# Kernel optimization log

Measured on AMD Instinct MI355X. Metric: run time of the kernel, lower is better.

## Reference

```python
import jax, jax.numpy as jnp
import numpy as np

N = 100000
E = 1600000


def _gcn_conv(x, src, dst, norm, W, b, n_nodes):
    # PyG GCNConv: h = x @ W; aggregate normalized messages; add bias.
    h = x @ W                                   # [N, C_out]
    msg = h[src] * norm[:, None]                # [E', C_out] gathered messages
    out = jax.ops.segment_sum(msg, dst, num_segments=n_nodes)
    return out + b


def _norm_coeffs(src, dst, n_nodes):
    # symmetric normalization with self-loops: D^{-1/2} (A+I) D^{-1/2}
    ones = jnp.ones(src.shape[0], dtype=jnp.float32)
    deg = jax.ops.segment_sum(ones, dst, num_segments=n_nodes)
    dis = jnp.where(deg > 0, jax.lax.rsqrt(jnp.maximum(deg, 1.0)), 0.0)
    return dis[src] * dis[dst]


def setup_inputs() -> dict:
    key = jax.random.key(0)
    k1, k2, k3, k4 = jax.random.split(key, 4)
    x = jax.random.normal(k1, (N, 128), dtype=jnp.float32)
    edge_index = jax.random.randint(k2, (2, E), 0, N, dtype=jnp.int64)
    W1 = jax.random.normal(k3, (128, 128), dtype=jnp.float32) * (1.0 / np.sqrt(128))
    b1 = jnp.zeros((128,), dtype=jnp.float32)
    W2 = jax.random.normal(k4, (128, 64), dtype=jnp.float32) * (1.0 / np.sqrt(128))
    b2 = jnp.zeros((64,), dtype=jnp.float32)
    return {"x": x, "edge_index": edge_index, "W1": W1, "b1": b1, "W2": W2, "b2": b2}


def reference(x, edge_index, W1, b1, W2, b2):
    n_nodes = x.shape[0]
    loop = jnp.arange(n_nodes, dtype=edge_index.dtype)
    src = jnp.concatenate([edge_index[0], loop])   # add self-loops
    dst = jnp.concatenate([edge_index[1], loop])
    norm = _norm_coeffs(src, dst, n_nodes)
    h = _gcn_conv(x, src, dst, norm, W1, b1, n_nodes)
    h = jax.nn.relu(h)
    # dropout(p=0.2) is identity in eval mode
    out = _gcn_conv(h, src, dst, norm, W2, b2, n_nodes)
    return out
```

## Files before the change

kernel.cpp:

```cpp
#include <hip/hip_runtime.h>
#include <hip/hip_bf16.h>


typedef short short8v __attribute__((ext_vector_type(8)));
typedef float f32x4   __attribute__((ext_vector_type(4)));
typedef int   int4v   __attribute__((ext_vector_type(4)));

#define BSHIFT 9
#define BSIZE  512
#define CAPSH  14
#define CAP    (1 << CAPSH)
#define IDXCAP 4096

__device__ __forceinline__ short f2bf(float f) {
    unsigned u = __float_as_uint(f);
    return (short)((u + 0x7fffu + ((u >> 16) & 1u)) >> 16);
}
__device__ __forceinline__ unsigned pack2bf(float a, float b) {
    return (unsigned)(unsigned short)f2bf(a) | ((unsigned)(unsigned short)f2bf(b) << 16);
}
__device__ __forceinline__ float bflo(unsigned u) { return __uint_as_float(u << 16); }
__device__ __forceinline__ float bfhi(unsigned u) { return __uint_as_float(u & 0xffff0000u); }

__global__ void k_prep(const float* __restrict__ W1, const float* __restrict__ W2,
                       short* __restrict__ w1t, short* __restrict__ w2t,
                       int* __restrict__ bcur, int nbuck,
                       short* __restrict__ bufH, short* __restrict__ bufH2, int N) {
    int b = blockIdx.x;
    int t = threadIdx.x;
    if (b == gridDim.x - 1) {
        if (t < nbuck) bcur[t] = t << CAPSH;
        size_t np1 = (size_t)N + 1;
        if (t < 128) {
            bufH[((size_t)(t >> 4) * np1 + N) * 16 + (t & 15)] = 0;
        } else if (t < 192) {
            int z = t - 128;
            bufH2[((size_t)(z >> 4) * np1 + N) * 16 + (z & 15)] = 0;
        }
        return;
    }
    int i = b * 256 + t;
    if (i < 128 * 128) {
        int n = i >> 7, k = i & 127;
        w1t[i] = f2bf(W1[k * 128 + n]);
    } else {
        int j = i - 128 * 128;
        int n = j >> 7, k = j & 127;
        w2t[j] = f2bf(W2[k * 64 + n]);
    }
}

__global__ __launch_bounds__(256) void k_bucket(const int* __restrict__ src,
                                                const int* __restrict__ dst,
                                                int* __restrict__ bcur,
                                                unsigned* __restrict__ ebuf,
                                                int E, int nbuck) {
    __shared__ int sdst[4096];
    __shared__ int ssrc[4096];
    __shared__ int hist[256];
    __shared__ int base[256];
    int t = threadIdx.x;
    int e0 = blockIdx.x * 4096;
    for (int i = t; i < nbuck; i += 256) hist[i] = 0;
    for (int i = 0; i < 16; ++i) {
        int k = i * 256 + t;
        int e = e0 + k;
        sdst[k] = (e < E) ? dst[e] : -1;
        ssrc[k] = (e < E) ? src[e] : 0;
    }
    __syncthreads();
    for (int i = 0; i < 16; ++i) {
        int d = sdst[i * 256 + t];
        if (d >= 0) atomicAdd(&hist[d >> BSHIFT], 1);
    }
    __syncthreads();
    for (int b = t; b < nbuck; b += 256) {
        int c = hist[b];
        base[b] = c ? atomicAdd(&bcur[b], c) : 0;
        hist[b] = 0;
    }
    __syncthreads();
    for (int i = 0; i < 16; ++i) {
        int k = i * 256 + t;
        int d = sdst[k];
        if (d >= 0) {
            int bk = d >> BSHIFT;
            int off = atomicAdd(&hist[bk], 1);
            ebuf[base[bk] + off] = ((unsigned)ssrc[k] << BSHIFT) | (unsigned)(d & (BSIZE - 1));
        }
    }
}

__global__ __launch_bounds__(BSIZE) void k_bcsr(const unsigned* __restrict__ ebuf,
                                                const int* __restrict__ bcur,
                                                float* __restrict__ dinv,
                                                int* __restrict__ nord,
                                                int* __restrict__ degr,
                                                int* __restrict__ rpr,
                                                unsigned* __restrict__ csr4, int n) {
    __shared__ unsigned edges[CAP];
    __shared__ int hist[BSIZE];
    __shared__ int s[BSIZE];
    __shared__ int cur[BSIZE];
    int b = blockIdx.x;
    int t = threadIdx.x;
    hist[t] = 0;
    __syncthreads();
    int base = b << CAPSH;
    int cnt  = bcur[b] - base;
    int lo = b << BSHIFT;
    for (int k = t; k < cnt; k += BSIZE) {
        unsigned e = ebuf[base + k];
        edges[k] = e;
        atomicAdd(&hist[e & (BSIZE - 1)], 1);
    }
    __syncthreads();
    int v = hist[t];
    int node = lo + t;
    bool valid = node < n;
    __syncthreads();
    hist[t] = 0;
    __syncthreads();
    int key = valid ? min(v, BSIZE - 1) : 0;
    atomicAdd(&hist[key], 1);
    __syncthreads();
    s[t] = hist[t];
    __syncthreads();
    for (int off = 1; off < BSIZE; off <<= 1) {
        int add = (t >= off) ? s[t - off] : 0;
        __syncthreads();
        s[t] += add;
        __syncthreads();
    }
    cur[t] = 0;
    __syncthreads();
    int r = (s[key] - hist[key]) + atomicAdd(&cur[key], 1);
    __syncthreads();
    int pv = valid ? ((v + 4) & ~3) : 0;
    s[r] = pv;
    __syncthreads();
    for (int off = 1; off < BSIZE; off <<= 1) {
        int add = (t >= off) ? s[t - off] : 0;
        __syncthreads();
        s[t] += add;
        __syncthreads();
    }
    int rp = base + s[r] - pv;
    cur[t] = rp + 1;
    int slot = (b << BSHIFT) + r;
    if (valid) {
        dinv[node] = rsqrtf((float)(v + 1));
        nord[slot] = node;
        degr[slot] = v;
        rpr[slot]  = rp;
        csr4[rp] = (unsigned)node;
        for (int j = v + 1; j < pv; ++j) csr4[rp + j] = (unsigned)n;
    } else {
        nord[slot] = -1;
        degr[slot] = 0;
        rpr[slot]  = rp;
    }
    __syncthreads();
    for (int k = t; k < cnt; k += BSIZE) {
        unsigned e = edges[k];
        int pos = atomicAdd(&cur[e & (BSIZE - 1)], 1);
        csr4[pos] = e >> BSHIFT;
    }
}

#define LDP 136
__global__ __launch_bounds__(256) void k_gemm1(const float* __restrict__ x,
                                               const short* __restrict__ w1t,
                                               const float* __restrict__ dinv,
                                               short* __restrict__ h, int nrows) {
    __shared__ short xs[64 * LDP];
    __shared__ short wt[128 * LDP];
    int t = threadIdx.x;
    int row0 = blockIdx.x * 64;
    for (int i = 0; i < 16; ++i) {
        int idx = t + i * 256;
        int r = idx >> 5, c4 = idx & 31;
        float4 v = make_float4(0.f, 0.f, 0.f, 0.f);
        if (row0 + r < nrows) v = ((const float4*)x)[(size_t)(row0 + r) * 32 + c4];
        short4 o = make_short4(f2bf(v.x), f2bf(v.y), f2bf(v.z), f2bf(v.w));
        *(short4*)&xs[r * LDP + c4 * 4] = o;
    }
    for (int i = 0; i < 16; ++i) {
        int idx = t + i * 256;
        int n = idx >> 5, c4 = idx & 31;
        *(short4*)&wt[n * LDP + c4 * 4] = ((const short4*)w1t)[idx];
    }
    __syncthreads();
    int wave = t >> 6, lane = t & 63;
    int quad = lane >> 4, c = lane & 15;
    int m0 = wave * 16;
    f32x4 acc[8] = {};
    #pragma unroll
    for (int kc = 0; kc < 4; ++kc) {
        short8v a = *(const short8v*)&xs[(m0 + c) * LDP + kc * 32 + quad * 8];
        #pragma unroll
        for (int nt = 0; nt < 8; ++nt) {
            short8v b = *(const short8v*)&wt[(nt * 16 + c) * LDP + kc * 32 + quad * 8];
            acc[nt] = __builtin_amdgcn_mfma_f32_16x16x32_bf16(a, b, acc[nt], 0, 0, 0);
        }
    }
    size_t slab = ((size_t)nrows + 1) * 16;
    #pragma unroll
    for (int r = 0; r < 4; ++r) {
        int row = row0 + m0 + quad * 4 + r;
        if (row < nrows) {
            float dr = dinv[row];
            #pragma unroll
            for (int nt = 0; nt < 8; ++nt)
                h[(size_t)nt * slab + (size_t)row * 16 + c] = f2bf(acc[nt][r] * dr);
        }
    }
}

__global__ __launch_bounds__(256) void k_gemm2(const unsigned* __restrict__ aggb,
                                               const float* __restrict__ b1,
                                               const short* __restrict__ w2t,
                                               const float* __restrict__ dinv,
                                               short* __restrict__ h2, int nrows) {
    __shared__ short xs[64 * LDP];
    __shared__ short wt[64 * LDP];
    int t = threadIdx.x;
    int row0 = blockIdx.x * 64;
    size_t slab8 = ((size_t)nrows + 1) * 8;
    for (int i = 0; i < 16; ++i) {
        int idx = t + i * 256;
        int r = idx >> 6, cp = idx & 63;
        unsigned o = 0;
        if (row0 + r < nrows) {
            unsigned u = aggb[(size_t)(cp >> 3) * slab8 + (size_t)(row0 + r) * 8 + (cp & 7)];
            float2 bb = ((const float2*)b1)[cp];
            float vx = fmaxf(bflo(u) + bb.x, 0.f);
            float vy = fmaxf(bfhi(u) + bb.y, 0.f);
            o = pack2bf(vx, vy);
        }
        *(unsigned*)&xs[r * LDP + cp * 2] = o;
    }
    for (int i = 0; i < 8; ++i) {
        int idx = t + i * 256;
        int n = idx >> 5, c4 = idx & 31;
        *(short4*)&wt[n * LDP + c4 * 4] = ((const short4*)w2t)[idx];
    }
    __syncthreads();
    int wave = t >> 6, lane = t & 63;
    int quad = lane >> 4, c = lane & 15;
    int m0 = wave * 16;
    f32x4 acc[4] = {};
    #pragma unroll
    for (int kc = 0; kc < 4; ++kc) {
        short8v av = *(const short8v*)&xs[(m0 + c) * LDP + kc * 32 + quad * 8];
        #pragma unroll
        for (int nt = 0; nt < 4; ++nt) {
            short8v b = *(const short8v*)&wt[(nt * 16 + c) * LDP + kc * 32 + quad * 8];
            acc[nt] = __builtin_amdgcn_mfma_f32_16x16x32_bf16(av, b, acc[nt], 0, 0, 0);
        }
    }
    size_t slab16 = ((size_t)nrows + 1) * 16;
    #pragma unroll
    for (int r = 0; r < 4; ++r) {
        int row = row0 + m0 + quad * 4 + r;
        if (row < nrows) {
            float dr = dinv[row];
            #pragma unroll
            for (int nt = 0; nt < 4; ++nt)
                h2[(size_t)nt * slab16 + (size_t)row * 16 + c] = f2bf(acc[nt][r] * dr);
        }
    }
}

__global__ __launch_bounds__(256) void k_pull128(const unsigned* __restrict__ h,
                                                 const int* __restrict__ nord,
                                                 const int* __restrict__ degr,
                                                 const int* __restrict__ rpr,
                                                 const unsigned* __restrict__ csr4,
                                                 unsigned* __restrict__ aggb,
                                                 int n) {
    __shared__ int sIdx[IDXCAP];
    __shared__ int sN[64];
    __shared__ int sV[64];
    __shared__ int sRP[64];
    int chunk = blockIdx.x & 7;
    int sb    = blockIdx.x >> 3;
    int s0 = sb * 64;
    int t = threadIdx.x;
    if (t < 64) {
        sN[t]  = __builtin_nontemporal_load(&nord[s0 + t]);
        sV[t]  = __builtin_nontemporal_load(&degr[s0 + t]);
        sRP[t] = __builtin_nontemporal_load(&rpr[s0 + t]);
    }
    __syncthreads();
    int rpBeg = sRP[0];
    int pvL = (sN[63] >= 0) ? ((sV[63] + 4) & ~3) : 0;
    int range = sRP[63] + pvL - rpBeg;
    bool fast = (range <= IDXCAP);
    if (fast) {
        for (int j = t * 4; j < range; j += 1024) {
            int4v vv = __builtin_nontemporal_load((const int4v*)(csr4 + rpBeg + j));
            *(int4v*)&sIdx[j] = vv;
        }
    }
    __syncthreads();

    int lane = t & 63;
    int wv   = t >> 6;
    int grp  = lane >> 2;
    int sub  = lane & 3;
    int li = wv * 16 + grp;
    int node = sN[li];
    bool alive = node >= 0;
    int v  = sV[li];
    int pv = alive ? ((v + 4) & ~3) : 0;
    int off = sRP[li] - rpBeg;
    const unsigned* hc = h + (size_t)chunk * (((size_t)n + 1) * 8);
    float a0 = 0.f, a1 = 0.f, a2 = 0.f, a3 = 0.f;
    if (fast) {
        for (int k = 0; k < pv; k += 4) {
            int o = off + k;
            int x0 = sIdx[o], x1 = sIdx[o + 1], x2 = sIdx[o + 2], x3 = sIdx[o + 3];
            uint2 g0 = *(const uint2*)&hc[(x0 << 3) + (sub << 1)];
            uint2 g1 = *(const uint2*)&hc[(x1 << 3) + (sub << 1)];
            uint2 g2 = *(const uint2*)&hc[(x2 << 3) + (sub << 1)];
            uint2 g3 = *(const uint2*)&hc[(x3 << 3) + (sub << 1)];
            a0 += bflo(g0.x); a1 += bfhi(g0.x); a2 += bflo(g0.y); a3 += bfhi(g0.y);
            a0 += bflo(g1.x); a1 += bfhi(g1.x); a2 += bflo(g1.y); a3 += bfhi(g1.y);
            a0 += bflo(g2.x); a1 += bfhi(g2.x); a2 += bflo(g2.y); a3 += bfhi(g2.y);
            a0 += bflo(g3.x); a1 += bfhi(g3.x); a2 += bflo(g3.y); a3 += bfhi(g3.y);
        }
    } else {
        for (int k = 0; k < pv; k += 4) {
            int o = rpBeg + off + k;
            int x0 = csr4[o], x1 = csr4[o + 1], x2 = csr4[o + 2], x3 = csr4[o + 3];
            uint2 g0 = *(const uint2*)&hc[(x0 << 3) + (sub << 1)];
            uint2 g1 = *(const uint2*)&hc[(x1 << 3) + (sub << 1)];
            uint2 g2 = *(const uint2*)&hc[(x2 << 3) + (sub << 1)];
            uint2 g3 = *(const uint2*)&hc[(x3 << 3) + (sub << 1)];
            a0 += bflo(g0.x); a1 += bfhi(g0.x); a2 += bflo(g0.y); a3 += bfhi(g0.y);
            a0 += bflo(g1.x); a1 += bfhi(g1.x); a2 += bflo(g1.y); a3 += bfhi(g1.y);
            a0 += bflo(g2.x); a1 += bfhi(g2.x); a2 += bflo(g2.y); a3 += bfhi(g2.y);
            a0 += bflo(g3.x); a1 += bfhi(g3.x); a2 += bflo(g3.y); a3 += bfhi(g3.y);
        }
    }
    if (alive) {
        float di = rsqrtf((float)(v + 1));
        unsigned* ab = aggb + (size_t)chunk * (((size_t)n + 1) * 8);
        uint2 o2;
        o2.x = pack2bf(a0 * di, a1 * di);
        o2.y = pack2bf(a2 * di, a3 * di);
        *(uint2*)&ab[(node << 3) + (sub << 1)] = o2;
    }
}

__global__ __launch_bounds__(256) void k_pull64(const unsigned* __restrict__ h2,
                                                const int* __restrict__ nord,
                                                const int* __restrict__ degr,
                                                const int* __restrict__ rpr,
                                                const unsigned* __restrict__ csr4,
                                                const float* __restrict__ b2,
                                                float* __restrict__ out, int n) {
    __shared__ int sIdx[IDXCAP];
    __shared__ int sN[64];
    __shared__ int sV[64];
    __shared__ int sRP[64];
    int chunk = blockIdx.x & 3;
    int sb    = blockIdx.x >> 2;
    int s0 = sb * 64;
    int t = threadIdx.x;
    if (t < 64) {
        sN[t]  = __builtin_nontemporal_load(&nord[s0 + t]);
        sV[t]  = __builtin_nontemporal_load(&degr[s0 + t]);
        sRP[t] = __builtin_nontemporal_load(&rpr[s0 + t]);
    }
    __syncthreads();
    int rpBeg = sRP[0];
    int pvL = (sN[63] >= 0) ? ((sV[63] + 4) & ~3) : 0;
    int range = sRP[63] + pvL - rpBeg;
    bool fast = (range <= IDXCAP);
    if (fast) {
        for (int j = t * 4; j < range; j += 1024) {
            int4v vv = __builtin_nontemporal_load((const int4v*)(csr4 + rpBeg + j));
            *(int4v*)&sIdx[j] = vv;
        }
    }
    __syncthreads();

    int lane = t & 63;
    int wv   = t >> 6;
    int grp  = lane >> 2;
    int sub  = lane & 3;
    int li = wv * 16 + grp;
    int node = sN[li];
    bool alive = node >= 0;
    int v  = sV[li];
    int pv = alive ? ((v + 4) & ~3) : 0;
    int off = sRP[li] - rpBeg;
    const unsigned* hc = h2 + (size_t)chunk * (((size_t)n + 1) * 8);
    float a0 = 0.f, a1 = 0.f, a2 = 0.f, a3 = 0.f;
    if (fast) {
        for (int k = 0; k < pv; k += 4) {
            int o = off + k;
            int x0 = sIdx[o], x1 = sIdx[o + 1], x2 = sIdx[o + 2], x3 = sIdx[o + 3];
            uint2 g0 = *(const uint2*)&hc[(x0 << 3) + (sub << 1)];
            uint2 g1 = *(const uint2*)&hc[(x1 << 3) + (sub << 1)];
            uint2 g2 = *(const uint2*)&hc[(x2 << 3) + (sub << 1)];
            uint2 g3 = *(const uint2*)&hc[(x3 << 3) + (sub << 1)];
            a0 += bflo(g0.x); a1 += bfhi(g0.x); a2 += bflo(g0.y); a3 += bfhi(g0.y);
            a0 += bflo(g1.x); a1 += bfhi(g1.x); a2 += bflo(g1.y); a3 += bfhi(g1.y);
            a0 += bflo(g2.x); a1 += bfhi(g2.x); a2 += bflo(g2.y); a3 += bfhi(g2.y);
            a0 += bflo(g3.x); a1 += bfhi(g3.x); a2 += bflo(g3.y); a3 += bfhi(g3.y);
        }
    } else {
        for (int k = 0; k < pv; k += 4) {
            int o = rpBeg + off + k;
            int x0 = csr4[o], x1 = csr4[o + 1], x2 = csr4[o + 2], x3 = csr4[o + 3];
            uint2 g0 = *(const uint2*)&hc[(x0 << 3) + (sub << 1)];
            uint2 g1 = *(const uint2*)&hc[(x1 << 3) + (sub << 1)];
            uint2 g2 = *(const uint2*)&hc[(x2 << 3) + (sub << 1)];
            uint2 g3 = *(const uint2*)&hc[(x3 << 3) + (sub << 1)];
            a0 += bflo(g0.x); a1 += bfhi(g0.x); a2 += bflo(g0.y); a3 += bfhi(g0.y);
            a0 += bflo(g1.x); a1 += bfhi(g1.x); a2 += bflo(g1.y); a3 += bfhi(g1.y);
            a0 += bflo(g2.x); a1 += bfhi(g2.x); a2 += bflo(g2.y); a3 += bfhi(g2.y);
            a0 += bflo(g3.x); a1 += bfhi(g3.x); a2 += bflo(g3.y); a3 += bfhi(g3.y);
        }
    }
    if (alive) {
        float di = rsqrtf((float)(v + 1));
        int f0 = chunk * 16 + sub * 4;
        float4 bb = *(const float4*)&b2[f0];
        float4 o;
        o.x = a0 * di + bb.x;
        o.y = a1 * di + bb.y;
        o.z = a2 * di + bb.z;
        o.w = a3 * di + bb.w;
        *(float4*)&out[(size_t)node * 64 + f0] = o;
    }
}

extern "C" void kernel_launch(void* const* d_in, const int* in_sizes, int n_in,
                              void* d_out, int out_size, void* d_ws, size_t ws_size,
                              hipStream_t stream) {
    const float* x  = (const float*)d_in[0];
    const int*   ei = (const int*)d_in[1];
    const float* W1 = (const float*)d_in[2];
    const float* b1 = (const float*)d_in[3];
    const float* W2 = (const float*)d_in[4];
    const float* b2 = (const float*)d_in[5];
    float* out = (float*)d_out;

    const int N = in_sizes[0] / 128;
    const int E = in_sizes[1] / 2;
    const int* src = ei;
    const int* dst = ei + E;
    const int nbuck = (N + BSIZE - 1) >> BSHIFT;
    const int nslot = nbuck << BSHIFT;
    const size_t capE = (size_t)nbuck << CAPSH;
    const size_t np1 = (size_t)N + 1;

    float* dinv     = (float*)d_ws;
    int*   bcur     = (int*)(dinv + N);
    int*   nord     = bcur + 256;
    int*   degr     = nord + nslot;
    int*   rpr      = degr + nslot;
    short* w1t      = (short*)(rpr + nslot);
    short* w2t      = w1t + 128 * 128;
    unsigned* csr4  = (unsigned*)(w2t + 64 * 128);
    short* bufH     = (short*)(csr4 + capE);
    short* bufH2    = bufH + 8 * np1 * 16;
    unsigned* aggb  = (unsigned*)(bufH2 + 4 * np1 * 16);
    unsigned* ebuf  = aggb;

    const int ntile = (E + 4095) / 4096;
    const int nsb = nslot / 64;

    k_prep<<<97, 256, 0, stream>>>(W1, W2, w1t, w2t, bcur, nbuck, bufH, bufH2, N);

    k_bucket<<<ntile, 256, 0, stream>>>(src, dst, bcur, ebuf, E, nbuck);
    k_bcsr<<<nbuck, BSIZE, 0, stream>>>(ebuf, bcur, dinv, nord, degr, rpr, csr4, N);

    k_gemm1<<<(N + 63) / 64, 256, 0, stream>>>(x, w1t, dinv, bufH, N);
    k_pull128<<<8 * nsb, 256, 0, stream>>>((const unsigned*)bufH, nord, degr, rpr, csr4, aggb, N);

    k_gemm2<<<(N + 63) / 64, 256, 0, stream>>>(aggb, b1, w2t, dinv, bufH2, N);
    k_pull64<<<4 * nsb, 256, 0, stream>>>((const unsigned*)bufH2, nord, degr, rpr, csr4, b2, out, N);
}
```

Before: 331.0 us.

## Persistent pull kernels with double-buffered CSR index prefetch and packed node metadata

The two aggregation kernels become persistent: a fixed grid of blocks strides over 64-node groups. Each block preloads metadata for all its groups and double-buffers the next group's CSR indices in shared memory while it gathers the current group. The three per-slot arrays (node, degree, row pointer) are packed into one int4 record. The gather loop is unrolled to 8 neighbors with two accumulator sets and vectorized index reads, and output stores are nontemporal. The aim is to hide index-load latency and cut launch/setup overhead. In exchange the shared index buffer halves to 2048 entries, so more groups may fall back to the slower global-index path.

```diff
diff --git a/kernel.cpp b/kernel.cpp
--- a/kernel.cpp
+++ b/kernel.cpp
@@ -5,12 +5,15 @@
 typedef short short8v __attribute__((ext_vector_type(8)));
 typedef float f32x4   __attribute__((ext_vector_type(4)));
 typedef int   int4v   __attribute__((ext_vector_type(4)));
+typedef unsigned uint2v __attribute__((ext_vector_type(2)));
 
 #define BSHIFT 9
 #define BSIZE  512
 #define CAPSH  14
 #define CAP    (1 << CAPSH)
-#define IDXCAP 4096
+#define IDXC2  2048
+#define MAXG128 9
+#define MAXG64  5
 
 __device__ __forceinline__ short f2bf(float f) {
     unsigned u = __float_as_uint(f);
@@ -94,9 +97,7 @@
 __global__ __launch_bounds__(BSIZE) void k_bcsr(const unsigned* __restrict__ ebuf,
                                                 const int* __restrict__ bcur,
                                                 float* __restrict__ dinv,
-                                                int* __restrict__ nord,
-                                                int* __restrict__ degr,
-                                                int* __restrict__ rpr,
+                                                int4v* __restrict__ meta4,
                                                 unsigned* __restrict__ csr4, int n) {
     __shared__ unsigned edges[CAP];
     __shared__ int hist[BSIZE];
@@ -148,17 +149,16 @@
     int rp = base + s[r] - pv;
     cur[t] = rp + 1;
     int slot = (b << BSHIFT) + r;
+    int4v m;
+    m.x = valid ? node : -1;
+    m.y = valid ? v : 0;
+    m.z = rp;
+    m.w = 0;
+    meta4[slot] = m;
     if (valid) {
         dinv[node] = rsqrtf((float)(v + 1));
-        nord[slot] = node;
-        degr[slot] = v;
-        rpr[slot]  = rp;
         csr4[rp] = (unsigned)node;
         for (int j = v + 1; j < pv; ++j) csr4[rp + j] = (unsigned)n;
-    } else {
-        nord[slot] = -1;
-        degr[slot] = 0;
-        rpr[slot]  = rp;
     }
     __syncthreads();
     for (int k = t; k < cnt; k += BSIZE) {
@@ -273,169 +273,236 @@
 }
 
 __global__ __launch_bounds__(256) void k_pull128(const unsigned* __restrict__ h,
-                                                 const int* __restrict__ nord,
-                                                 const int* __restrict__ degr,
-                                                 const int* __restrict__ rpr,
+                                                 const int4v* __restrict__ meta4,
                                                  const unsigned* __restrict__ csr4,
                                                  unsigned* __restrict__ aggb,
-                                                 int n) {
-    __shared__ int sIdx[IDXCAP];
-    __shared__ int sN[64];
-    __shared__ int sV[64];
-    __shared__ int sRP[64];
+                                                 int n, int ngroups) {
+    __shared__ int sIdx[2][IDXC2];
+    __shared__ int4v sMeta[MAXG128 * 64];
     int chunk = blockIdx.x & 7;
-    int sb    = blockIdx.x >> 3;
-    int s0 = sb * 64;
-    int t = threadIdx.x;
-    if (t < 64) {
-        sN[t]  = __builtin_nontemporal_load(&nord[s0 + t]);
-        sV[t]  = __builtin_nontemporal_load(&degr[s0 + t]);
-        sRP[t] = __builtin_nontemporal_load(&rpr[s0 + t]);
-    }
-    __syncthreads();
-    int rpBeg = sRP[0];
-    int pvL = (sN[63] >= 0) ? ((sV[63] + 4) & ~3) : 0;
-    int range = sRP[63] + pvL - rpBeg;
-    bool fast = (range <= IDXCAP);
-    if (fast) {
-        for (int j = t * 4; j < range; j += 1024) {
-            int4v vv = __builtin_nontemporal_load((const int4v*)(csr4 + rpBeg + j));
-            *(int4v*)&sIdx[j] = vv;
-        }
-    }
-    __syncthreads();
-
-    int lane = t & 63;
-    int wv   = t >> 6;
-    int grp  = lane >> 2;
-    int sub  = lane & 3;
+    int nbsl  = gridDim.x >> 3;
+    int bsl   = blockIdx.x >> 3;
+    int t = threadIdx.x;
+    if (bsl >= ngroups) return;
+    int gcount = (ngroups - bsl + nbsl - 1) / nbsl;
+    for (int u = t; u < gcount * 64; u += 256) {
+        int gi = u >> 6, li = u & 63;
+        int sg = bsl + gi * nbsl;
+        sMeta[u] = __builtin_nontemporal_load(&meta4[(size_t)sg * 64 + li]);
+    }
+    __syncthreads();
+
+    const unsigned* hc = h + (size_t)chunk * (((size_t)n + 1) * 8);
+    unsigned* ab = aggb + (size_t)chunk * (((size_t)n + 1) * 8);
+    int lane = t & 63, wv = t >> 6;
+    int grp = lane >> 2, sub = lane & 3;
     int li = wv * 16 + grp;
-    int node = sN[li];
-    bool alive = node >= 0;
-    int v  = sV[li];
-    int pv = alive ? ((v + 4) & ~3) : 0;
-    int off = sRP[li] - rpBeg;
-    const unsigned* hc = h + (size_t)chunk * (((size_t)n + 1) * 8);
-    float a0 = 0.f, a1 = 0.f, a2 = 0.f, a3 = 0.f;
-    if (fast) {
-        for (int k = 0; k < pv; k += 4) {
-            int o = off + k;
-            int x0 = sIdx[o], x1 = sIdx[o + 1], x2 = sIdx[o + 2], x3 = sIdx[o + 3];
-            uint2 g0 = *(const uint2*)&hc[(x0 << 3) + (sub << 1)];
-            uint2 g1 = *(const uint2*)&hc[(x1 << 3) + (sub << 1)];
-            uint2 g2 = *(const uint2*)&hc[(x2 << 3) + (sub << 1)];
-            uint2 g3 = *(const uint2*)&hc[(x3 << 3) + (sub << 1)];
-            a0 += bflo(g0.x); a1 += bfhi(g0.x); a2 += bflo(g0.y); a3 += bfhi(g0.y);
-            a0 += bflo(g1.x); a1 += bfhi(g1.x); a2 += bflo(g1.y); a3 += bfhi(g1.y);
-            a0 += bflo(g2.x); a1 += bfhi(g2.x); a2 += bflo(g2.y); a3 += bfhi(g2.y);
-            a0 += bflo(g3.x); a1 += bfhi(g3.x); a2 += bflo(g3.y); a3 += bfhi(g3.y);
-        }
-    } else {
-        for (int k = 0; k < pv; k += 4) {
-            int o = rpBeg + off + k;
-            int x0 = csr4[o], x1 = csr4[o + 1], x2 = csr4[o + 2], x3 = csr4[o + 3];
-            uint2 g0 = *(const uint2*)&hc[(x0 << 3) + (sub << 1)];
-            uint2 g1 = *(const uint2*)&hc[(x1 << 3) + (sub << 1)];
-            uint2 g2 = *(const uint2*)&hc[(x2 << 3) + (sub << 1)];
-            uint2 g3 = *(const uint2*)&hc[(x3 << 3) + (sub << 1)];
-            a0 += bflo(g0.x); a1 += bfhi(g0.x); a2 += bflo(g0.y); a3 += bfhi(g0.y);
-            a0 += bflo(g1.x); a1 += bfhi(g1.x); a2 += bflo(g1.y); a3 += bfhi(g1.y);
-            a0 += bflo(g2.x); a1 += bfhi(g2.x); a2 += bflo(g2.y); a3 += bfhi(g2.y);
-            a0 += bflo(g3.x); a1 += bfhi(g3.x); a2 += bflo(g3.y); a3 += bfhi(g3.y);
-        }
-    }
-    if (alive) {
-        float di = rsqrtf((float)(v + 1));
-        unsigned* ab = aggb + (size_t)chunk * (((size_t)n + 1) * 8);
-        uint2 o2;
-        o2.x = pack2bf(a0 * di, a1 * di);
-        o2.y = pack2bf(a2 * di, a3 * di);
-        *(uint2*)&ab[(node << 3) + (sub << 1)] = o2;
+
+    {
+        int4v m0 = sMeta[0], mL = sMeta[63];
+        int rpBeg = m0.z;
+        int pvL = (mL.x >= 0) ? ((mL.y + 4) & ~3) : 0;
+        int range = mL.z + pvL - rpBeg;
+        if (range <= IDXC2)
+            for (int j = t * 4; j < range; j += 1024)
+                *(int4v*)&sIdx[0][j] = __builtin_nontemporal_load((const int4v*)(csr4 + rpBeg + j));
+    }
+    int cur = 0;
+    for (int gi = 0; gi < gcount; ++gi) {
+        __syncthreads();
+        if (gi + 1 < gcount) {
+            int4v m0 = sMeta[(gi + 1) * 64], mL = sMeta[(gi + 1) * 64 + 63];
+            int rpBeg = m0.z;
+            int pvL = (mL.x >= 0) ? ((mL.y + 4) & ~3) : 0;
+            int range = mL.z + pvL - rpBeg;
+            if (range <= IDXC2)
+                for (int j = t * 4; j < range; j += 1024)
+                    *(int4v*)&sIdx[cur ^ 1][j] = __builtin_nontemporal_load((const int4v*)(csr4 + rpBeg + j));
+        }
+        int4v m  = sMeta[gi * 64 + li];
+        int4v m0 = sMeta[gi * 64], mL = sMeta[gi * 64 + 63];
+        int rpBeg = m0.z;
+        int pvL = (mL.x >= 0) ? ((mL.y + 4) & ~3) : 0;
+        bool fast = (mL.z + pvL - rpBeg) <= IDXC2;
+        int node = m.x, v = m.y;
+        int pv = (node >= 0) ? ((v + 4) & ~3) : 0;
+        float a0 = 0.f, a1 = 0.f, a2 = 0.f, a3 = 0.f;
+        float c0 = 0.f, c1 = 0.f, c2 = 0.f, c3 = 0.f;
+        if (fast) {
+            const int* ip = &sIdx[cur][m.z - rpBeg];
+            int k = 0;
+            for (; k + 8 <= pv; k += 8) {
+                int4v q0 = *(const int4v*)(ip + k);
+                int4v q1 = *(const int4v*)(ip + k + 4);
+                uint2v g0 = *(const uint2v*)&hc[(q0.x << 3) + (sub << 1)];
+                uint2v g1 = *(const uint2v*)&hc[(q0.y << 3) + (sub << 1)];
+                uint2v g2 = *(const uint2v*)&hc[(q0.z << 3) + (sub << 1)];
+                uint2v g3 = *(const uint2v*)&hc[(q0.w << 3) + (sub << 1)];
+                uint2v g4 = *(const uint2v*)&hc[(q1.x << 3) + (sub << 1)];
+                uint2v g5 = *(const uint2v*)&hc[(q1.y << 3) + (sub << 1)];
+                uint2v g6 = *(const uint2v*)&hc[(q1.z << 3) + (sub << 1)];
+                uint2v g7 = *(const uint2v*)&hc[(q1.w << 3) + (sub << 1)];
+                a0 += bflo(g0[0]); a1 += bfhi(g0[0]); a2 += bflo(g0[1]); a3 += bfhi(g0[1]);
+                a0 += bflo(g1[0]); a1 += bfhi(g1[0]); a2 += bflo(g1[1]); a3 += bfhi(g1[1]);
+                a0 += bflo(g2[0]); a1 += bfhi(g2[0]); a2 += bflo(g2[1]); a3 += bfhi(g2[1]);
+                a0 += bflo(g3[0]); a1 += bfhi(g3[0]); a2 += bflo(g3[1]); a3 += bfhi(g3[1]);
+                c0 += bflo(g4[0]); c1 += bfhi(g4[0]); c2 += bflo(g4[1]); c3 += bfhi(g4[1]);
+                c0 += bflo(g5[0]); c1 += bfhi(g5[0]); c2 += bflo(g5[1]); c3 += bfhi(g5[1]);
+                c0 += bflo(g6[0]); c1 += bfhi(g6[0]); c2 += bflo(g6[1]); c3 += bfhi(g6[1]);
+                c0 += bflo(g7[0]); c1 += bfhi(g7[0]); c2 += bflo(g7[1]); c3 += bfhi(g7[1]);
+            }
+            if (k < pv) {
+                int4v q = *(const int4v*)(ip + k);
+                uint2v g0 = *(const uint2v*)&hc[(q.x << 3) + (sub << 1)];
+                uint2v g1 = *(const uint2v*)&hc[(q.y << 3) + (sub << 1)];
+                uint2v g2 = *(const uint2v*)&hc[(q.z << 3) + (sub << 1)];
+                uint2v g3 = *(const uint2v*)&hc[(q.w << 3) + (sub << 1)];
+                a0 += bflo(g0[0]); a1 += bfhi(g0[0]); a2 += bflo(g0[1]); a3 += bfhi(g0[1]);
+                a0 += bflo(g1[0]); a1 += bfhi(g1[0]); a2 += bflo(g1[1]); a3 += bfhi(g1[1]);
+                a0 += bflo(g2[0]); a1 += bfhi(g2[0]); a2 += bflo(g2[1]); a3 += bfhi(g2[1]);
+                a0 += bflo(g3[0]); a1 += bfhi(g3[0]); a2 += bflo(g3[1]); a3 += bfhi(g3[1]);
+            }
+        } else {
+            const unsigned* gp = csr4 + m.z;
+            for (int k = 0; k < pv; k += 4) {
+                int4v q = *(const int4v*)(gp + k);
+                uint2v g0 = *(const uint2v*)&hc[(q.x << 3) + (sub << 1)];
+                uint2v g1 = *(const uint2v*)&hc[(q.y << 3) + (sub << 1)];
+                uint2v g2 = *(const uint2v*)&hc[(q.z << 3) + (sub << 1)];
+                uint2v g3 = *(const uint2v*)&hc[(q.w << 3) + (sub << 1)];
+                a0 += bflo(g0[0]); a1 += bfhi(g0[0]); a2 += bflo(g0[1]); a3 += bfhi(g0[1]);
+                a0 += bflo(g1[0]); a1 += bfhi(g1[0]); a2 += bflo(g1[1]); a3 += bfhi(g1[1]);
+                a0 += bflo(g2[0]); a1 += bfhi(g2[0]); a2 += bflo(g2[1]); a3 += bfhi(g2[1]);
+                a0 += bflo(g3[0]); a1 += bfhi(g3[0]); a2 += bflo(g3[1]); a3 += bfhi(g3[1]);
+            }
+        }
+        if (node >= 0) {
+            float di = rsqrtf((float)(v + 1));
+            a0 += c0; a1 += c1; a2 += c2; a3 += c3;
+            uint2v o2;
+            o2[0] = pack2bf(a0 * di, a1 * di);
+            o2[1] = pack2bf(a2 * di, a3 * di);
+            __builtin_nontemporal_store(o2, (uint2v*)&ab[((size_t)node << 3) + (sub << 1)]);
+        }
+        cur ^= 1;
     }
 }
 
 __global__ __launch_bounds__(256) void k_pull64(const unsigned* __restrict__ h2,
-                                                const int* __restrict__ nord,
-                                                const int* __restrict__ degr,
-                                                const int* __restrict__ rpr,
+                                                const int4v* __restrict__ meta4,
                                                 const unsigned* __restrict__ csr4,
                                                 const float* __restrict__ b2,
-                                                float* __restrict__ out, int n) {
-    __shared__ int sIdx[IDXCAP];
-    __shared__ int sN[64];
-    __shared__ int sV[64];
-    __shared__ int sRP[64];
+                                                float* __restrict__ out, int n, int ngroups) {
+    __shared__ int sIdx[2][IDXC2];
+    __shared__ int4v sMeta[MAXG64 * 64];
     int chunk = blockIdx.x & 3;
-    int sb    = blockIdx.x >> 2;
-    int s0 = sb * 64;
-    int t = threadIdx.x;
-    if (t < 64) {
-        sN[t]  = __builtin_nontemporal_load(&nord[s0 + t]);
-        sV[t]  = __builtin_nontemporal_load(&degr[s0 + t]);
-        sRP[t] = __builtin_nontemporal_load(&rpr[s0 + t]);
-    }
-    __syncthreads();
-    int rpBeg = sRP[0];
-    int pvL = (sN[63] >= 0) ? ((sV[63] + 4) & ~3) : 0;
-    int range = sRP[63] + pvL - rpBeg;
-    bool fast = (range <= IDXCAP);
-    if (fast) {
-        for (int j = t * 4; j < range; j += 1024) {
-            int4v vv = __builtin_nontemporal_load((const int4v*)(csr4 + rpBeg + j));
-            *(int4v*)&sIdx[j] = vv;
-        }
-    }
-    __syncthreads();
-
-    int lane = t & 63;
-    int wv   = t >> 6;
-    int grp  = lane >> 2;
-    int sub  = lane & 3;
+    int nbsl  = gridDim.x >> 2;
+    int bsl   = blockIdx.x >> 2;
+    int t = threadIdx.x;
+    if (bsl >= ngroups) return;
+    int gcount = (ngroups - bsl + nbsl - 1) / nbsl;
+    for (int u = t; u < gcount * 64; u += 256) {
+        int gi = u >> 6, li = u & 63;
+        int sg = bsl + gi * nbsl;
+        sMeta[u] = __builtin_nontemporal_load(&meta4[(size_t)sg * 64 + li]);
+    }
+    __syncthreads();
+
+    const unsigned* hc = h2 + (size_t)chunk * (((size_t)n + 1) * 8);
+    int lane = t & 63, wv = t >> 6;
+    int grp = lane >> 2, sub = lane & 3;
     int li = wv * 16 + grp;
-    int node = sN[li];
-    bool alive = node >= 0;
-    int v  = sV[li];
-    int pv = alive ? ((v + 4) & ~3) : 0;
-    int off = sRP[li] - rpBeg;
-    const unsigned* hc = h2 + (size_t)chunk * (((size_t)n + 1) * 8);
-    float a0 = 0.f, a1 = 0.f, a2 = 0.f, a3 = 0.f;
-    if (fast) {
-        for (int k = 0; k < pv; k += 4) {
-            int o = off + k;
-            int x0 = sIdx[o], x1 = sIdx[o + 1], x2 = sIdx[o + 2], x3 = sIdx[o + 3];
-            uint2 g0 = *(const uint2*)&hc[(x0 << 3) + (sub << 1)];
-            uint2 g1 = *(const uint2*)&hc[(x1 << 3) + (sub << 1)];
-            uint2 g2 = *(const uint2*)&hc[(x2 << 3) + (sub << 1)];
-            uint2 g3 = *(const uint2*)&hc[(x3 << 3) + (sub << 1)];
-            a0 += bflo(g0.x); a1 += bfhi(g0.x); a2 += bflo(g0.y); a3 += bfhi(g0.y);
-            a0 += bflo(g1.x); a1 += bfhi(g1.x); a2 += bflo(g1.y); a3 += bfhi(g1.y);
-            a0 += bflo(g2.x); a1 += bfhi(g2.x); a2 += bflo(g2.y); a3 += bfhi(g2.y);
-            a0 += bflo(g3.x); a1 += bfhi(g3.x); a2 += bflo(g3.y); a3 += bfhi(g3.y);
-        }
-    } else {
-        for (int k = 0; k < pv; k += 4) {
-            int o = rpBeg + off + k;
-            int x0 = csr4[o], x1 = csr4[o + 1], x2 = csr4[o + 2], x3 = csr4[o + 3];
-            uint2 g0 = *(const uint2*)&hc[(x0 << 3) + (sub << 1)];
-            uint2 g1 = *(const uint2*)&hc[(x1 << 3) + (sub << 1)];
-            uint2 g2 = *(const uint2*)&hc[(x2 << 3) + (sub << 1)];
-            uint2 g3 = *(const uint2*)&hc[(x3 << 3) + (sub << 1)];
-            a0 += bflo(g0.x); a1 += bfhi(g0.x); a2 += bflo(g0.y); a3 += bfhi(g0.y);
-            a0 += bflo(g1.x); a1 += bfhi(g1.x); a2 += bflo(g1.y); a3 += bfhi(g1.y);
-            a0 += bflo(g2.x); a1 += bfhi(g2.x); a2 += bflo(g2.y); a3 += bfhi(g2.y);
-            a0 += bflo(g3.x); a1 += bfhi(g3.x); a2 += bflo(g3.y); a3 += bfhi(g3.y);
-        }
-    }
-    if (alive) {
-        float di = rsqrtf((float)(v + 1));
-        int f0 = chunk * 16 + sub * 4;
-        float4 bb = *(const float4*)&b2[f0];
-        float4 o;
-        o.x = a0 * di + bb.x;
-        o.y = a1 * di + bb.y;
-        o.z = a2 * di + bb.z;
-        o.w = a3 * di + bb.w;
-        *(float4*)&out[(size_t)node * 64 + f0] = o;
+    f32x4 bb = *(const f32x4*)&b2[chunk * 16 + sub * 4];
+
+    {
+        int4v m0 = sMeta[0], mL = sMeta[63];
+        int rpBeg = m0.z;
+        int pvL = (mL.x >= 0) ? ((mL.y + 4) & ~3) : 0;
+        int range = mL.z + pvL - rpBeg;
+        if (range <= IDXC2)
+            for (int j = t * 4; j < range; j += 1024)
+                *(int4v*)&sIdx[0][j] = __builtin_nontemporal_load((const int4v*)(csr4 + rpBeg + j));
+    }
+    int cur = 0;
+    for (int gi = 0; gi < gcount; ++gi) {
+        __syncthreads();
+        if (gi + 1 < gcount) {
+            int4v m0 = sMeta[(gi + 1) * 64], mL = sMeta[(gi + 1) * 64 + 63];
+            int rpBeg = m0.z;
+            int pvL = (mL.x >= 0) ? ((mL.y + 4) & ~3) : 0;
+            int range = mL.z + pvL - rpBeg;
+            if (range <= IDXC2)
+                for (int j = t * 4; j < range; j += 1024)
+                    *(int4v*)&sIdx[cur ^ 1][j] = __builtin_nontemporal_load((const int4v*)(csr4 + rpBeg + j));
+        }
+        int4v m  = sMeta[gi * 64 + li];
+        int4v m0 = sMeta[gi * 64], mL = sMeta[gi * 64 + 63];
+        int rpBeg = m0.z;
+        int pvL = (mL.x >= 0) ? ((mL.y + 4) & ~3) : 0;
+        bool fast = (mL.z + pvL - rpBeg) <= IDXC2;
+        int node = m.x, v = m.y;
+        int pv = (node >= 0) ? ((v + 4) & ~3) : 0;
+        float a0 = 0.f, a1 = 0.f, a2 = 0.f, a3 = 0.f;
+        float c0 = 0.f, c1 = 0.f, c2 = 0.f, c3 = 0.f;
+        if (fast) {
+            const int* ip = &sIdx[cur][m.z - rpBeg];
+            int k = 0;
+            for (; k + 8 <= pv; k += 8) {
+                int4v q0 = *(const int4v*)(ip + k);
+                int4v q1 = *(const int4v*)(ip + k + 4);
+                uint2v g0 = *(const uint2v*)&hc[(q0.x << 3) + (sub << 1)];
+                uint2v g1 = *(const uint2v*)&hc[(q0.y << 3) + (sub << 1)];
+                uint2v g2 = *(const uint2v*)&hc[(q0.z << 3) + (sub << 1)];
+                uint2v g3 = *(const uint2v*)&hc[(q0.w << 3) + (sub << 1)];
+                uint2v g4 = *(const uint2v*)&hc[(q1.x << 3) + (sub << 1)];
+                uint2v g5 = *(const uint2v*)&hc[(q1.y << 3) + (sub << 1)];
+                uint2v g6 = *(const uint2v*)&hc[(q1.z << 3) + (sub << 1)];
+                uint2v g7 = *(const uint2v*)&hc[(q1.w << 3) + (sub << 1)];
+                a0 += bflo(g0[0]); a1 += bfhi(g0[0]); a2 += bflo(g0[1]); a3 += bfhi(g0[1]);
+                a0 += bflo(g1[0]); a1 += bfhi(g1[0]); a2 += bflo(g1[1]); a3 += bfhi(g1[1]);
+                a0 += bflo(g2[0]); a1 += bfhi(g2[0]); a2 += bflo(g2[1]); a3 += bfhi(g2[1]);
+                a0 += bflo(g3[0]); a1 += bfhi(g3[0]); a2 += bflo(g3[1]); a3 += bfhi(g3[1]);
+                c0 += bflo(g4[0]); c1 += bfhi(g4[0]); c2 += bflo(g4[1]); c3 += bfhi(g4[1]);
+                c0 += bflo(g5[0]); c1 += bfhi(g5[0]); c2 += bflo(g5[1]); c3 += bfhi(g5[1]);
+                c0 += bflo(g6[0]); c1 += bfhi(g6[0]); c2 += bflo(g6[1]); c3 += bfhi(g6[1]);
+                c0 += bflo(g7[0]); c1 += bfhi(g7[0]); c2 += bflo(g7[1]); c3 += bfhi(g7[1]);
+            }
+            if (k < pv) {
+                int4v q = *(const int4v*)(ip + k);
+                uint2v g0 = *(const uint2v*)&hc[(q.x << 3) + (sub << 1)];
+                uint2v g1 = *(const uint2v*)&hc[(q.y << 3) + (sub << 1)];
+                uint2v g2 = *(const uint2v*)&hc[(q.z << 3) + (sub << 1)];
+                uint2v g3 = *(const uint2v*)&hc[(q.w << 3) + (sub << 1)];
+                a0 += bflo(g0[0]); a1 += bfhi(g0[0]); a2 += bflo(g0[1]); a3 += bfhi(g0[1]);
+                a0 += bflo(g1[0]); a1 += bfhi(g1[0]); a2 += bflo(g1[1]); a3 += bfhi(g1[1]);
+                a0 += bflo(g2[0]); a1 += bfhi(g2[0]); a2 += bflo(g2[1]); a3 += bfhi(g2[1]);
+                a0 += bflo(g3[0]); a1 += bfhi(g3[0]); a2 += bflo(g3[1]); a3 += bfhi(g3[1]);
+            }
+        } else {
+            const unsigned* gp = csr4 + m.z;
+            for (int k = 0; k < pv; k += 4) {
+                int4v q = *(const int4v*)(gp + k);
+                uint2v g0 = *(const uint2v*)&hc[(q.x << 3) + (sub << 1)];
+                uint2v g1 = *(const uint2v*)&hc[(q.y << 3) + (sub << 1)];
+                uint2v g2 = *(const uint2v*)&hc[(q.z << 3) + (sub << 1)];
+                uint2v g3 = *(const uint2v*)&hc[(q.w << 3) + (sub << 1)];
+                a0 += bflo(g0[0]); a1 += bfhi(g0[0]); a2 += bflo(g0[1]); a3 += bfhi(g0[1]);
+                a0 += bflo(g1[0]); a1 += bfhi(g1[0]); a2 += bflo(g1[1]); a3 += bfhi(g1[1]);
+                a0 += bflo(g2[0]); a1 += bfhi(g2[0]); a2 += bflo(g2[1]); a3 += bfhi(g2[1]);
+                a0 += bflo(g3[0]); a1 += bfhi(g3[0]); a2 += bflo(g3[1]); a3 += bfhi(g3[1]);
+            }
+        }
+        if (node >= 0) {
+            float di = rsqrtf((float)(v + 1));
+            a0 += c0; a1 += c1; a2 += c2; a3 += c3;
+            f32x4 o;
+            o[0] = a0 * di + bb[0];
+            o[1] = a1 * di + bb[1];
+            o[2] = a2 * di + bb[2];
+            o[3] = a3 * di + bb[3];
+            __builtin_nontemporal_store(o, (f32x4*)&out[(size_t)node * 64 + chunk * 16 + sub * 4]);
+        }
+        cur ^= 1;
     }
 }
 
@@ -456,15 +523,14 @@
     const int* dst = ei + E;
     const int nbuck = (N + BSIZE - 1) >> BSHIFT;
     const int nslot = nbuck << BSHIFT;
+    const int ngroups = nslot >> 6;
     const size_t capE = (size_t)nbuck << CAPSH;
     const size_t np1 = (size_t)N + 1;
 
     float* dinv     = (float*)d_ws;
     int*   bcur     = (int*)(dinv + N);
-    int*   nord     = bcur + 256;
-    int*   degr     = nord + nslot;
-    int*   rpr      = degr + nslot;
-    short* w1t      = (short*)(rpr + nslot);
+    int4v* meta4    = (int4v*)(bcur + 256);
+    short* w1t      = (short*)(meta4 + nslot);
     short* w2t      = w1t + 128 * 128;
     unsigned* csr4  = (unsigned*)(w2t + 64 * 128);
     short* bufH     = (short*)(csr4 + capE);
@@ -473,16 +539,20 @@
     unsigned* ebuf  = aggb;
 
     const int ntile = (E + 4095) / 4096;
-    const int nsb = nslot / 64;
+
+    int nbsl1 = 192;
+    if ((ngroups + nbsl1 - 1) / nbsl1 > MAXG128) nbsl1 = (ngroups + MAXG128 - 1) / MAXG128;
+    int nbsl2 = 384;
+    if ((ngroups + nbsl2 - 1) / nbsl2 > MAXG64)  nbsl2 = (ngroups + MAXG64 - 1) / MAXG64;
 
     k_prep<<<97, 256, 0, stream>>>(W1, W2, w1t, w2t, bcur, nbuck, bufH, bufH2, N);
 
     k_bucket<<<ntile, 256, 0, stream>>>(src, dst, bcur, ebuf, E, nbuck);
-    k_bcsr<<<nbuck, BSIZE, 0, stream>>>(ebuf, bcur, dinv, nord, degr, rpr, csr4, N);
+    k_bcsr<<<nbuck, BSIZE, 0, stream>>>(ebuf, bcur, dinv, meta4, csr4, N);
 
     k_gemm1<<<(N + 63) / 64, 256, 0, stream>>>(x, w1t, dinv, bufH, N);
-    k_pull128<<<8 * nsb, 256, 0, stream>>>((const unsigned*)bufH, nord, degr, rpr, csr4, aggb, N);
+    k_pull128<<<8 * nbsl1, 256, 0, stream>>>((const unsigned*)bufH, meta4, csr4, aggb, N, ngroups);
 
     k_gemm2<<<(N + 63) / 64, 256, 0, stream>>>(aggb, b1, w2t, dinv, bufH2, N);
-    k_pull64<<<4 * nsb, 256, 0, stream>>>((const unsigned*)bufH2, nord, degr, rpr, csr4, b2, out, N);
-}
+    k_pull64<<<4 * nbsl2, 256, 0, stream>>>((const unsigned*)bufH2, meta4, csr4, b2, out, N, ngroups);
+}
```

Measured after the change: 347.6 us. 5.0% more time.
